# Performance work log

Measured on AMD Instinct MI355X. Metric: run time of the kernel, lower is better.

The kernel has to match this reference:

```python
import jax, jax.numpy as jnp
import numpy as np
from jax import lax

N_POINTS = 4096
D_FEAT = 64


def setup_inputs() -> dict:
    key = jax.random.key(0)
    x = jax.random.normal(key, (N_POINTS, D_FEAT), dtype=jnp.float32)
    return {"x": x}


def _pairwise_dist(x):
    # Euclidean distance matrix [n, n]; diagonal masked to +inf so a point
    # never pairs with itself. Diagonal of D2 is set to 1.0 (not 0) before
    # sqrt so the backward pass is NaN-free.
    sq = jnp.sum(x * x, axis=1)
    D2 = sq[:, None] + sq[None, :] - 2.0 * (x @ x.T)
    n = x.shape[0]
    eye = jnp.eye(n, dtype=bool)
    D2 = jnp.where(eye, 1.0, jnp.maximum(D2, 1e-12))
    D = jnp.sqrt(D2)
    return jnp.where(eye, jnp.inf, D)


def _h0_flag_diagram(D):
    # Dim-0 persistence of the Rips (flag) filtration: every vertex is born at
    # filtration value 0; the n-1 finite deaths are exactly the edge lengths of
    # the minimum spanning tree of the distance graph. Computed with Prim's
    # algorithm vectorized over the frontier (one lax.scan step per MST edge).
    n = D.shape[0]
    intree0 = jnp.zeros((n,), dtype=bool).at[0].set(True)
    mind0 = D[0]  # min distance from the tree to each vertex

    def step(carry, _):
        mind, intree = carry
        masked = jnp.where(intree, jnp.inf, mind)
        j = jnp.argmin(masked)          # next vertex merged into the tree
        death = masked[j]               # edge length at which its class dies
        intree = intree.at[j].set(True)
        mind = jnp.minimum(mind, D[j])
        return (mind, intree), death

    _, deaths = lax.scan(step, (mind0, intree0), None, length=n - 1)
    births = jnp.zeros_like(deaths)
    return jnp.stack([births, deaths], axis=1)  # [n-1, 2]


def reference(x):
    D = _pairwise_dist(x)
    dgm0 = _h0_flag_diagram(D)
    return dgm0
```

## Files before the change

kernel.cpp:

```cpp
#include <hip/hip_runtime.h>
#include <math.h>


#define N 4096
#define DF 64
#define INF __builtin_huge_valf()

__global__ __launch_bounds__(256) void build_d_kernel(const float* __restrict__ x,
                                                      float* __restrict__ D,
                                                      unsigned long long* __restrict__ best) {
    __shared__ float As[64][68];
    __shared__ float Bs[64][68];
    const int bi = blockIdx.y * 64;
    const int bj = blockIdx.x * 64;
    const int t = threadIdx.x;

#pragma unroll
    for (int g = 0; g < 4; ++g) {
        int idx = t + 256 * g;
        int row = idx >> 4;
        int k4 = (idx & 15) << 2;
        *(float4*)(&As[row][k4]) = *(const float4*)(x + (size_t)(bi + row) * DF + k4);
        *(float4*)(&Bs[row][k4]) = *(const float4*)(x + (size_t)(bj + row) * DF + k4);
    }
    __syncthreads();

    const int ti = (t >> 4) << 2;
    const int tj = (t & 15) << 2;
    float acc[4][4];
#pragma unroll
    for (int r = 0; r < 4; ++r)
#pragma unroll
        for (int c = 0; c < 4; ++c) acc[r][c] = 0.0f;

    for (int k = 0; k < 64; k += 4) {
        float4 a[4], b[4];
#pragma unroll
        for (int r = 0; r < 4; ++r) a[r] = *(const float4*)(&As[ti + r][k]);
#pragma unroll
        for (int c = 0; c < 4; ++c) b[c] = *(const float4*)(&Bs[tj + c][k]);
#pragma unroll
        for (int r = 0; r < 4; ++r)
#pragma unroll
            for (int c = 0; c < 4; ++c) {
                float d0 = a[r].x - b[c].x;
                float d1 = a[r].y - b[c].y;
                float d2 = a[r].z - b[c].z;
                float d3 = a[r].w - b[c].w;
                float s = acc[r][c];
                s = fmaf(d0, d0, s);
                s = fmaf(d1, d1, s);
                s = fmaf(d2, d2, s);
                s = fmaf(d3, d3, s);
                acc[r][c] = s;
            }
    }
#pragma unroll
    for (int r = 0; r < 4; ++r) {
        int i = bi + ti + r;
        float4 v;
        float* vp = &v.x;
        unsigned long long mk = ~0ULL;
#pragma unroll
        for (int c = 0; c < 4; ++c) {
            int j = bj + tj + c;
            vp[c] = (i == j) ? INF : sqrtf(fmaxf(acc[r][c], 1e-12f));
            unsigned long long key =
                ((unsigned long long)__float_as_uint(vp[c]) << 24) |
                ((unsigned long long)(unsigned)i << 12) | (unsigned)j;
            mk = key < mk ? key : mk;
        }
        *(float4*)(D + (size_t)i * N + (bj + tj)) = v;
#pragma unroll
        for (int m = 1; m < 16; m <<= 1) {
            unsigned long long o = __shfl_xor(mk, m, 64);
            mk = o < mk ? o : mk;
        }
        if ((t & 15) == 0) atomicMin(&best[i], mk);
    }
}

__global__ __launch_bounds__(256) void init_kernel(unsigned* comp,
                                                   unsigned long long* best,
                                                   unsigned* nedges, unsigned* done) {
    int i = blockIdx.x * 256 + threadIdx.x;
    if (i < N) {
        comp[i] = (unsigned)i;
        best[i] = ~0ULL;
    }
    if (i == 0) { *nedges = 0u; *done = 0u; }
}

__global__ __launch_bounds__(256) void minedge_d_kernel(const float* __restrict__ D,
                                                        const unsigned* __restrict__ comp,
                                                        unsigned long long* __restrict__ best,
                                                        const unsigned* __restrict__ done) {
    if (*done) return;
    __shared__ unsigned compc[N];
    __shared__ unsigned long long keybuf[256];
    const int t = threadIdx.x;
    const int b = blockIdx.x;
    const int r = t >> 4;
    const int j = t & 15;
    const int rowv = b * 16 + r;

    for (int v = t; v < N; v += 256) compc[v] = comp[v];
    __syncthreads();
    const unsigned cr = compc[rowv];
    const float4* rowp = (const float4*)(D + (size_t)rowv * N);
    unsigned long long mykey = ~0ULL;
#pragma unroll 4
    for (int k = 0; k < 64; ++k) {
        float4 v4 = rowp[j + 16 * k];
        int c0 = 4 * (j + 16 * k);
        const float* vp = &v4.x;
#pragma unroll
        for (int q = 0; q < 4; ++q) {
            int c = c0 + q;
            if (compc[c] != cr) {
                unsigned long long key =
                    ((unsigned long long)__float_as_uint(vp[q]) << 24) |
                    ((unsigned long long)(unsigned)rowv << 12) | (unsigned)c;
                mykey = key < mykey ? key : mykey;
            }
        }
    }
    keybuf[t] = mykey;
    __syncthreads();
    if (t < 16) {
        unsigned long long k = ~0ULL;
#pragma unroll
        for (int i = 0; i < 16; ++i) {
            unsigned long long v2 = keybuf[t * 16 + i];
            k = v2 < k ? v2 : k;
        }
        if (k != ~0ULL) atomicMin(&best[compc[b * 16 + t]], k);
    }
}

__global__ __launch_bounds__(256) void minedge_kernel(const float* __restrict__ x,
                                                      const unsigned* __restrict__ comp,
                                                      unsigned long long* __restrict__ best,
                                                      const unsigned* __restrict__ done) {
    if (*done) return;
    __shared__ float xr[16][64];
    __shared__ float xc[64][68];
    __shared__ unsigned compr[16];
    __shared__ unsigned compc[64];
    __shared__ unsigned long long keybuf[256];
    const int t = threadIdx.x;
    const int b = blockIdx.x;
    const int r = t >> 4;
    const int rowv = b * 16 + r;

    {
        int row = t >> 4, f4 = t & 15;
        *(float4*)&xr[row][f4 * 4] =
            *(const float4*)(x + (size_t)(b * 16 + row) * DF + f4 * 4);
        if (t < 16) compr[t] = comp[b * 16 + t];
    }
    __syncthreads();
    const unsigned cr = compr[r];
    unsigned long long mykey = ~0ULL;

    for (int tile = 0; tile < 64; ++tile) {
        {
#pragma unroll
            for (int q = 0; q < 4; ++q) {
                int idx = t + 256 * q;
                int col = idx >> 4, k4 = (idx & 15) * 4;
                *(float4*)&xc[col][k4] =
                    *(const float4*)(x + (size_t)(tile * 64 + col) * DF + k4);
            }
            if (t < 64) compc[t] = comp[tile * 64 + t];
        }
        __syncthreads();
#pragma unroll
        for (int q = 0; q < 4; ++q) {
            int c = (t & 15) + 16 * q;
            unsigned cc = compc[c];
            if (cc != cr) {
                float s = 0.0f;
#pragma unroll
                for (int k = 0; k < 64; k += 4) {
                    float4 a = *(const float4*)&xr[r][k];
                    float4 bb = *(const float4*)&xc[c][k];
                    float d0 = a.x - bb.x;
                    float d1 = a.y - bb.y;
                    float d2 = a.z - bb.z;
                    float d3 = a.w - bb.w;
                    s = fmaf(d0, d0, s);
                    s = fmaf(d1, d1, s);
                    s = fmaf(d2, d2, s);
                    s = fmaf(d3, d3, s);
                }
                float w = sqrtf(fmaxf(s, 1e-12f));
                unsigned long long key =
                    ((unsigned long long)__float_as_uint(w) << 24) |
                    ((unsigned long long)(unsigned)rowv << 12) |
                    (unsigned)(tile * 64 + c);
                mykey = key < mykey ? key : mykey;
            }
        }
        __syncthreads();
    }
    keybuf[t] = mykey;
    __syncthreads();
    if (t < 16) {
        unsigned long long k = ~0ULL;
#pragma unroll
        for (int i = 0; i < 16; ++i) {
            unsigned long long v2 = keybuf[t * 16 + i];
            k = v2 < k ? v2 : k;
        }
        if (k != ~0ULL) atomicMin(&best[compr[t]], k);
    }
}

__global__ void merge_kernel(unsigned* comp, unsigned long long* best,
                             unsigned long long* edges, unsigned* nedges,
                             unsigned* done) {
    if (*done) return;
    __shared__ unsigned cl[N];
    __shared__ unsigned np[N];
    __shared__ unsigned cnt;
    const int t = threadIdx.x;
    const int bs = blockDim.x;
    for (int v = t; v < N; v += bs) cl[v] = comp[v];
    __syncthreads();
    for (int v = t; v < N; v += bs) {
        unsigned p;
        if (cl[v] == (unsigned)v) {
            unsigned long long k = best[v];
            p = (k != ~0ULL) ? cl[(unsigned)(k & 0xFFFu)] : (unsigned)v;
        } else {
            p = cl[v];
        }
        np[v] = p;
    }
    __syncthreads();
    for (int v = t; v < N; v += bs) {
        if (cl[v] == (unsigned)v) {
            unsigned p = np[v];
            if (p != (unsigned)v) {
                bool mutual = (np[p] == (unsigned)v);
                if (mutual && (unsigned)v < p) {
                    np[v] = (unsigned)v;
                } else {
                    unsigned idx = atomicAdd(nedges, 1u);
                    edges[idx] = best[v];
                }
            }
        }
    }
    __syncthreads();
    for (int it = 0; it < 12; ++it) {
        for (int v = t; v < N; v += bs) np[v] = np[np[v]];
        __syncthreads();
    }
    if (t == 0) cnt = 0;
    __syncthreads();
    unsigned local = 0;
    for (int v = t; v < N; v += bs) {
        comp[v] = np[v];
        best[v] = ~0ULL;
        if (np[v] == (unsigned)v) ++local;
    }
    atomicAdd(&cnt, local);
    __syncthreads();
    if (t == 0 && cnt == 1u) *done = 1u;
}

__global__ __launch_bounds__(1024) void replay_kernel(
        const unsigned long long* __restrict__ edges,
        const unsigned* __restrict__ nedges, float* __restrict__ out) {
    __shared__ __align__(16) unsigned char pool[156680];
    __shared__ unsigned chg;
    unsigned* off = (unsigned*)(pool + 65536);
    unsigned long long* ent = (unsigned long long*)(pool + 0);
    unsigned short* par = (unsigned short*)(pool + 81928);
    unsigned* keyw = (unsigned*)(pool + 90120);
    unsigned long long* key64 = (unsigned long long*)(pool + 0);
    unsigned long long* order = (unsigned long long*)(pool + 0);
    unsigned* ptr = (unsigned*)(pool + 106504);
    unsigned short* rankA = (unsigned short*)(pool + 106504);
    unsigned short* nxtA = (unsigned short*)(pool + 122888);
    unsigned short* twin = (unsigned short*)(pool + 139272);
    unsigned* Sa = (unsigned*)(pool + 32768);
    unsigned* Sb = (unsigned*)(pool + 49152);
    unsigned* T = (unsigned*)(pool + 65536);
    unsigned* vA = (unsigned*)(pool + 122888);
    unsigned* jA = (unsigned*)(pool + 139272);
    unsigned* vB = (unsigned*)(pool + 0);
    unsigned* jB = (unsigned*)(pool + 16384);
    unsigned* csum = (unsigned*)(pool + 155656);
    const int t = threadIdx.x;
    const unsigned ne = *nedges;
    const int ns = 2 * (int)ne;

    for (int v = t; v < N; v += 1024) off[v] = 0u;
    if (t == 0) off[N] = 0u;
    for (int k = t; k < N - 1; k += 1024) out[2 * k] = 0.0f;
    __syncthreads();
    for (int e = t; e < (int)ne; e += 1024) {
        unsigned long long k = edges[e];
        atomicAdd(&off[(unsigned)(k >> 12) & 0xFFFu], 1u);
        atomicAdd(&off[(unsigned)k & 0xFFFu], 1u);
    }
    __syncthreads();
    unsigned sloc = 0;
    unsigned loc[16];
    if (t < 256) {
        int base = t * 16;
#pragma unroll
        for (int i = 0; i < 16; ++i) {
            unsigned d = off[base + i];
            loc[i] = sloc;
            sloc += d;
        }
        csum[t] = sloc;
    }
    __syncthreads();
    for (int d = 1; d < 256; d <<= 1) {
        unsigned addv = 0;
        if (t < 256 && t >= d) addv = csum[t - d];
        __syncthreads();
        if (t < 256) csum[t] += addv;
        __syncthreads();
    }
    if (t < 256) {
        int base = t * 16;
        unsigned excl = csum[t] - sloc;
#pragma unroll
        for (int i = 0; i < 16; ++i) {
            unsigned o = loc[i] + excl;
            off[base + i] = o;
            keyw[base + i] = o;
        }
        if (t == 255) off[N] = csum[255];
    }
    __syncthreads();
    for (int e = t; e < (int)ne; e += 1024) {
        unsigned long long k = edges[e];
        unsigned a = (unsigned)(k >> 12) & 0xFFFu;
        unsigned b = (unsigned)k & 0xFFFu;
        unsigned long long wb = k >> 24;
        unsigned p1 = atomicAdd(&keyw[a], 1u);
        unsigned p2 = atomicAdd(&keyw[b], 1u);
        ent[p1] = (wb << 12) | b;
        ent[p2] = (wb << 12) | a;
        twin[p1] = (unsigned short)p2;
        twin[p2] = (unsigned short)p1;
    }
    __syncthreads();
    const unsigned s0 = off[0];
    for (int s = t; s < ns; s += 1024) {
        unsigned v = (unsigned)ent[s] & 0xFFFu;
        unsigned t2 = twin[s];
        unsigned nx = t2 + 1u;
        if (nx == off[v + 1]) nx = off[v];
        if (nx == s0) nx = 0xFFFFu;
        nxtA[s] = (unsigned short)nx;
        rankA[s] = 1;
    }
    __syncthreads();
    for (int round = 0; round < 14; ++round) {
        unsigned short rr[8], nn[8];
#pragma unroll
        for (int q = 0; q < 8; ++q) {
            int s = t + 1024 * q;
            rr[q] = 0;
            nn[q] = 0xFFFFu;
            if (s < ns) {
                unsigned n2 = nxtA[s];
                if (n2 != 0xFFFFu) {
                    rr[q] = rankA[n2];
                    nn[q] = nxtA[n2];
                } else {
                    nn[q] = 0xFFFFu;
                }
            }
        }
        __syncthreads();
#pragma unroll
        for (int q = 0; q < 8; ++q) {
            int s = t + 1024 * q;
            if (s < ns) {
                if (nxtA[s] != 0xFFFFu) {
                    rankA[s] = (unsigned short)(rankA[s] + rr[q]);
                    nxtA[s] = nn[q];
                }
            }
        }
        __syncthreads();
    }
    for (int s = t; s < ns; s += 1024) {
        unsigned t2 = twin[s];
        if (rankA[s] > rankA[t2]) {
            unsigned v = (unsigned)ent[s] & 0xFFFu;
            par[v] = (unsigned short)((unsigned)ent[t2] & 0xFFFu);
            keyw[v] = (unsigned)(ent[s] >> 12);
        }
    }
    if (t == 0) {
        par[0] = 0;
        chg = 0u;
    }
    __syncthreads();
    for (int v = t; v < N; v += 1024) {
        key64[v] = (v == 0) ? ~0ULL
                            : (((unsigned long long)keyw[v]) << 24) |
                                  ((unsigned long long)par[v] << 12) | (unsigned)v;
    }
    __syncthreads();
    for (int v = t; v < N; v += 1024) ptr[v] = (v == 0) ? 0u : (unsigned)par[v];
    __syncthreads();
    for (;;) {
        for (int v = t; v < N; v += 1024) {
            unsigned p = ptr[v];
            if (key64[p] <= key64[v]) {
                unsigned q = ptr[p];
                if (q != p) {
                    ptr[v] = q;
                    chg = 1u;
                }
            }
        }
        __syncthreads();
        unsigned fin = (chg == 0u);
        __syncthreads();
        if (t == 0) chg = 0u;
        __syncthreads();
        if (fin) break;
    }
    unsigned* Sc = Sa;
    unsigned* Sn = Sb;
    for (int v = t; v < N; v += 1024) Sc[v] = 1u;
    __syncthreads();
    for (int round = 0; round < 64; ++round) {
        for (int v = t; v < N; v += 1024) Sn[v] = 1u;
        __syncthreads();
        for (int v = t; v < N; v += 1024)
            if (v != 0) atomicAdd(&Sn[ptr[v]], Sc[v]);
        __syncthreads();
        for (int v = t; v < N; v += 1024)
            if (Sn[v] != Sc[v]) chg = 1u;
        __syncthreads();
        unsigned fin = (chg == 0u);
        __syncthreads();
        if (t == 0) chg = 0u;
        __syncthreads();
        unsigned* tmp = Sc; Sc = Sn; Sn = tmp;
        if (fin) break;
    }
    for (int v = t; v < N; v += 1024) {
        order[v] = (v == 0)
                       ? (0xFFFFFull << 44)
                       : (((unsigned long long)ptr[v]) << 44) |
                             (((unsigned long long)keyw[v]) << 12) | (unsigned)v;
    }
    __syncthreads();
    for (unsigned k = 2; k <= 4096; k <<= 1) {
        for (unsigned j = k >> 1; j > 0; j >>= 1) {
            for (unsigned i = t; i < 4096; i += 1024) {
                unsigned p = i ^ j;
                if (p > i) {
                    unsigned long long a = order[i], b = order[p];
                    bool up = ((i & k) == 0);
                    if ((a > b) == up) {
                        order[i] = b;
                        order[p] = a;
                    }
                }
            }
            __syncthreads();
        }
    }
    for (int i = t; i < 4096; i += 1024) {
        unsigned vv = (unsigned)order[i] & 0xFFFu;
        T[i] = Sc[vv];
    }
    __syncthreads();
    for (int d = 1; d < 4096; d <<= 1) {
        unsigned addv[4];
#pragma unroll
        for (int q = 0; q < 4; ++q) {
            int i = t + 1024 * q;
            addv[q] = 0;
            if (i >= d && (order[i] >> 44) == (order[i - d] >> 44)) addv[q] = T[i - d];
        }
        __syncthreads();
#pragma unroll
        for (int q = 0; q < 4; ++q) T[t + 1024 * q] += addv[q];
        __syncthreads();
    }
    for (int i = t; i < 4096; i += 1024) {
        unsigned vv = (unsigned)order[i] & 0xFFFu;
        if (vv) {
            vA[vv] = 1u + T[i] - Sc[vv];
            jA[vv] = ptr[vv];
        }
    }
    if (t == 0) {
        vA[0] = 0u;
        jA[0] = 0u;
    }
    __syncthreads();
    {
        unsigned *va = vA, *vb = vB, *ja = jA, *jb = jB;
        for (int r = 0; r < 12; ++r) {
            for (int v = t; v < N; v += 1024) {
                unsigned j2 = ja[v];
                vb[v] = va[v] + va[j2];
                jb[v] = ja[j2];
            }
            __syncthreads();
            unsigned* tmp;
            tmp = va; va = vb; vb = tmp;
            tmp = ja; ja = jb; jb = tmp;
        }
        for (int v = t; v < N; v += 1024) {
            if (v) out[2 * (va[v] - 1) + 1] = __uint_as_float(keyw[v]);
        }
    }
}

extern "C" void kernel_launch(void* const* d_in, const int* in_sizes, int n_in,
                              void* d_out, int out_size, void* d_ws, size_t ws_size,
                              hipStream_t stream) {
    const float* x = (const float*)d_in[0];
    float* out = (float*)d_out;
    const size_t dbytes = (size_t)N * N * 4;

    if (ws_size >= dbytes + 81920) {
        float* D = (float*)d_ws;
        unsigned char* st = (unsigned char*)d_ws + dbytes;
        unsigned long long* best = (unsigned long long*)st;
        unsigned* comp = (unsigned*)(st + 32768);
        unsigned long long* edges = (unsigned long long*)(st + 49152);
        unsigned* nedges = (unsigned*)(st + 81912);
        unsigned* done = (unsigned*)(st + 81916);

        dim3 grid(N / 64, N / 64);
        init_kernel<<<16, 256, 0, stream>>>(comp, best, nedges, done);
        build_d_kernel<<<grid, 256, 0, stream>>>(x, D, best);
        merge_kernel<<<1, 1024, 0, stream>>>(comp, best, edges, nedges, done);
        for (int r = 1; r < 12; ++r) {
            minedge_d_kernel<<<256, 256, 0, stream>>>(D, comp, best, done);
            merge_kernel<<<1, 1024, 0, stream>>>(comp, best, edges, nedges, done);
        }
        replay_kernel<<<1, 1024, 0, stream>>>(edges, nedges, out);
    } else {
        unsigned char* ws = (unsigned char*)d_ws;
        unsigned* comp = (unsigned*)ws;
        unsigned long long* best = (unsigned long long*)(ws + 16384);
        unsigned long long* edges = (unsigned long long*)(ws + 49152);
        unsigned* nedges = (unsigned*)(ws + 81920);
        unsigned* done = (unsigned*)(ws + 81984);

        init_kernel<<<16, 256, 0, stream>>>(comp, best, nedges, done);
        for (int r = 0; r < 12; ++r) {
            minedge_kernel<<<256, 256, 0, stream>>>(x, comp, best, done);
            merge_kernel<<<1, 1024, 0, stream>>>(comp, best, edges, nedges, done);
        }
        replay_kernel<<<1, 1024, 0, stream>>>(edges, nedges, out);
    }
}
```

Measured before the change: 491.5 us.

## Fuse Boruvka min-edge search and merge into one kernel via last-block ticket

Replaces the separate minedge_d and merge kernel pair in each Boruvka round with a single 1024-thread kernel. Each wavefront scans one D row and the last block to arrive, detected with an atomic ticket counter, does the component merge: hooking, pointer jumping and resetting best. This removes one kernel launch per round and the single-block merge launch overhead. The price is a serial merge tail inside the last block, plus threadfence and atomic-visibility requirements. The replay kernel's list-ranking loop also drops from 14 to 13 rounds.

```diff
diff --git a/kernel.cpp b/kernel.cpp
--- a/kernel.cpp
+++ b/kernel.cpp
@@ -5,6 +5,10 @@
 #define N 4096
 #define DF 64
 #define INF __builtin_huge_valf()
+
+__device__ __forceinline__ unsigned long long aload64(const unsigned long long* p) {
+    return __hip_atomic_load(p, __ATOMIC_RELAXED, __HIP_MEMORY_SCOPE_AGENT);
+}
 
 __global__ __launch_bounds__(256) void build_d_kernel(const float* __restrict__ x,
                                                       float* __restrict__ D,
@@ -82,60 +86,123 @@
 
 __global__ __launch_bounds__(256) void init_kernel(unsigned* comp,
                                                    unsigned long long* best,
-                                                   unsigned* nedges, unsigned* done) {
+                                                   unsigned* nedges, unsigned* done,
+                                                   unsigned* counter) {
     int i = blockIdx.x * 256 + threadIdx.x;
     if (i < N) {
         comp[i] = (unsigned)i;
         best[i] = ~0ULL;
     }
-    if (i == 0) { *nedges = 0u; *done = 0u; }
-}
-
-__global__ __launch_bounds__(256) void minedge_d_kernel(const float* __restrict__ D,
-                                                        const unsigned* __restrict__ comp,
-                                                        unsigned long long* __restrict__ best,
-                                                        const unsigned* __restrict__ done) {
+    if (i == 0) { *nedges = 0u; *done = 0u; *counter = 0u; }
+}
+
+__global__ __launch_bounds__(1024) void minedge_merge_kernel(
+        const float* __restrict__ D, unsigned* comp, unsigned long long* best,
+        unsigned long long* edges, unsigned* nedges, unsigned* done,
+        unsigned* counter) {
     if (*done) return;
     __shared__ unsigned compc[N];
-    __shared__ unsigned long long keybuf[256];
+    __shared__ unsigned np[N];
+    __shared__ unsigned ticket_sh, cnt_sh;
     const int t = threadIdx.x;
     const int b = blockIdx.x;
-    const int r = t >> 4;
-    const int j = t & 15;
-    const int rowv = b * 16 + r;
-
-    for (int v = t; v < N; v += 256) compc[v] = comp[v];
-    __syncthreads();
-    const unsigned cr = compc[rowv];
-    const float4* rowp = (const float4*)(D + (size_t)rowv * N);
-    unsigned long long mykey = ~0ULL;
+    const int wv = t >> 6, lane = t & 63;
+
+    for (int v = t; v < N; v += 1024) compc[v] = comp[v];
+    __syncthreads();
+
+    {
+        const int rowv = b * 16 + wv;
+        const unsigned cr = compc[rowv];
+        const float4* rowp = (const float4*)(D + (size_t)rowv * N);
+        unsigned long long mykey = ~0ULL;
 #pragma unroll 4
-    for (int k = 0; k < 64; ++k) {
-        float4 v4 = rowp[j + 16 * k];
-        int c0 = 4 * (j + 16 * k);
-        const float* vp = &v4.x;
-#pragma unroll
-        for (int q = 0; q < 4; ++q) {
-            int c = c0 + q;
-            if (compc[c] != cr) {
-                unsigned long long key =
-                    ((unsigned long long)__float_as_uint(vp[q]) << 24) |
-                    ((unsigned long long)(unsigned)rowv << 12) | (unsigned)c;
-                mykey = key < mykey ? key : mykey;
-            }
-        }
-    }
-    keybuf[t] = mykey;
-    __syncthreads();
-    if (t < 16) {
+        for (int k = 0; k < 16; ++k) {
+            float4 v4 = rowp[lane + 64 * k];
+            int c0 = 4 * (lane + 64 * k);
+            uint4 cc4 = *(const uint4*)&compc[c0];
+            const float* vp = &v4.x;
+            const unsigned* cp = &cc4.x;
+#pragma unroll
+            for (int q = 0; q < 4; ++q) {
+                if (cp[q] != cr) {
+                    unsigned long long key =
+                        ((unsigned long long)__float_as_uint(vp[q]) << 24) |
+                        ((unsigned long long)(unsigned)rowv << 12) |
+                        (unsigned)(c0 + q);
+                    mykey = key < mykey ? key : mykey;
+                }
+            }
+        }
+#pragma unroll
+        for (int off = 32; off > 0; off >>= 1) {
+            unsigned long long o = __shfl_down(mykey, (unsigned)off, 64);
+            mykey = o < mykey ? o : mykey;
+        }
+        if (lane == 0 && mykey != ~0ULL) atomicMin(&best[cr], mykey);
+    }
+    __threadfence();
+    __syncthreads();
+    if (t == 0) ticket_sh = atomicAdd(counter, 1u);
+    __syncthreads();
+    if (ticket_sh != 255u) return;
+
+    if (t == 0) *counter = 0u;
+    unsigned long long kreg[4];
+#pragma unroll
+    for (int i = 0; i < 4; ++i) {
+        int v = t + 1024 * i;
+        unsigned p;
         unsigned long long k = ~0ULL;
-#pragma unroll
-        for (int i = 0; i < 16; ++i) {
-            unsigned long long v2 = keybuf[t * 16 + i];
-            k = v2 < k ? v2 : k;
-        }
-        if (k != ~0ULL) atomicMin(&best[compc[b * 16 + t]], k);
-    }
+        if (compc[v] == (unsigned)v) {
+            k = aload64(&best[v]);
+            p = (k != ~0ULL) ? compc[(unsigned)(k & 0xFFFu)] : (unsigned)v;
+        } else {
+            p = compc[v];
+        }
+        np[v] = p;
+        kreg[i] = k;
+    }
+    __syncthreads();
+#pragma unroll
+    for (int i = 0; i < 4; ++i) {
+        int v = t + 1024 * i;
+        if (compc[v] == (unsigned)v) {
+            unsigned p = np[v];
+            if (p != (unsigned)v) {
+                bool mutual = (np[p] == (unsigned)v);
+                if (mutual && (unsigned)v < p) {
+                    np[v] = (unsigned)v;
+                } else {
+                    unsigned idx = atomicAdd(nedges, 1u);
+                    edges[idx] = kreg[i];
+                }
+            }
+        }
+    }
+    __syncthreads();
+    for (int it = 0; it < 12; ++it) {
+#pragma unroll
+        for (int i = 0; i < 4; ++i) {
+            int v = t + 1024 * i;
+            np[v] = np[np[v]];
+        }
+        __syncthreads();
+    }
+    if (t == 0) cnt_sh = 0u;
+    __syncthreads();
+    unsigned local = 0;
+#pragma unroll
+    for (int i = 0; i < 4; ++i) {
+        int v = t + 1024 * i;
+        unsigned r2 = np[v];
+        comp[v] = r2;
+        best[v] = ~0ULL;
+        if (r2 == (unsigned)v) ++local;
+    }
+    atomicAdd(&cnt_sh, local);
+    __syncthreads();
+    if (t == 0 && cnt_sh == 1u) *done = 1u;
 }
 
 __global__ __launch_bounds__(256) void minedge_kernel(const float* __restrict__ x,
@@ -364,7 +431,7 @@
         rankA[s] = 1;
     }
     __syncthreads();
-    for (int round = 0; round < 14; ++round) {
+    for (int round = 0; round < 13; ++round) {
         unsigned short rr[8], nn[8];
 #pragma unroll
         for (int q = 0; q < 8; ++q) {
@@ -376,8 +443,6 @@
                 if (n2 != 0xFFFFu) {
                     rr[q] = rankA[n2];
                     nn[q] = nxtA[n2];
-                } else {
-                    nn[q] = 0xFFFFu;
                 }
             }
         }
@@ -385,11 +450,9 @@
 #pragma unroll
         for (int q = 0; q < 8; ++q) {
             int s = t + 1024 * q;
-            if (s < ns) {
-                if (nxtA[s] != 0xFFFFu) {
-                    rankA[s] = (unsigned short)(rankA[s] + rr[q]);
-                    nxtA[s] = nn[q];
-                }
+            if (s < ns && nxtA[s] != 0xFFFFu) {
+                rankA[s] = (unsigned short)(rankA[s] + rr[q]);
+                nxtA[s] = nn[q];
             }
         }
         __syncthreads();
@@ -532,7 +595,7 @@
     float* out = (float*)d_out;
     const size_t dbytes = (size_t)N * N * 4;
 
-    if (ws_size >= dbytes + 81920) {
+    if (ws_size >= dbytes + 90112) {
         float* D = (float*)d_ws;
         unsigned char* st = (unsigned char*)d_ws + dbytes;
         unsigned long long* best = (unsigned long long*)st;
@@ -540,14 +603,15 @@
         unsigned long long* edges = (unsigned long long*)(st + 49152);
         unsigned* nedges = (unsigned*)(st + 81912);
         unsigned* done = (unsigned*)(st + 81916);
+        unsigned* counter = (unsigned*)(st + 81920);
 
         dim3 grid(N / 64, N / 64);
-        init_kernel<<<16, 256, 0, stream>>>(comp, best, nedges, done);
+        init_kernel<<<16, 256, 0, stream>>>(comp, best, nedges, done, counter);
         build_d_kernel<<<grid, 256, 0, stream>>>(x, D, best);
         merge_kernel<<<1, 1024, 0, stream>>>(comp, best, edges, nedges, done);
         for (int r = 1; r < 12; ++r) {
-            minedge_d_kernel<<<256, 256, 0, stream>>>(D, comp, best, done);
-            merge_kernel<<<1, 1024, 0, stream>>>(comp, best, edges, nedges, done);
+            minedge_merge_kernel<<<256, 1024, 0, stream>>>(D, comp, best, edges,
+                                                           nedges, done, counter);
         }
         replay_kernel<<<1, 1024, 0, stream>>>(edges, nedges, out);
     } else {
@@ -558,7 +622,8 @@
         unsigned* nedges = (unsigned*)(ws + 81920);
         unsigned* done = (unsigned*)(ws + 81984);
 
-        init_kernel<<<16, 256, 0, stream>>>(comp, best, nedges, done);
+        init_kernel<<<16, 256, 0, stream>>>(comp, best, nedges, done,
+                                            (unsigned*)(ws + 81988));
         for (int r = 0; r < 12; ++r) {
             minedge_kernel<<<256, 256, 0, stream>>>(x, comp, best, done);
             merge_kernel<<<1, 1024, 0, stream>>>(comp, best, edges, nedges, done);
```

Measured after the change: 577.1 us. 1.17x slower.
